# Kernel optimization log

Measured on AMD Instinct MI355X. Metric: run time of the kernel, lower is better.

Reference implementation:

```python
import jax, jax.numpy as jnp
import numpy as np

B, N, DIM = 4, 1024, 512
H, DH = 8, 64
INNER = H * DH
MLP = 2048
EPS = 1e-5


def layernorm(x, g, b):
    m = x.mean(-1, keepdims=True)
    v = ((x - m) ** 2).mean(-1, keepdims=True)
    return (x - m) / jnp.sqrt(v + EPS) * g + b


def setup_inputs() -> dict:
    key = jax.random.key(0)
    ks = jax.random.split(key, 12)
    s = 0.02
    return {
        "q": jax.random.normal(ks[0], (B, N, DIM), jnp.float32),
        "k": jax.random.normal(ks[1], (B, N, DIM), jnp.float32),
        "v": jax.random.normal(ks[2], (B, N, DIM), jnp.float32),
        "Win": jax.random.normal(ks[3], (INNER, DIM), jnp.float32) * s,
        "Wout": jax.random.normal(ks[4], (DIM, INNER), jnp.float32) * s,
        "bout": jnp.zeros((DIM,), jnp.float32),
        "g1": jnp.ones((DIM,), jnp.float32),
        "b1n": jnp.zeros((DIM,), jnp.float32),
        "g2": jnp.ones((DIM,), jnp.float32),
        "b2n": jnp.zeros((DIM,), jnp.float32),
        "Wup": jax.random.normal(ks[5], (MLP, DIM), jnp.float32) * s,
        "bup": jnp.zeros((MLP,), jnp.float32),
        "Wdn": jax.random.normal(ks[6], (DIM, MLP), jnp.float32) * s,
        "bdn": jnp.zeros((DIM,), jnp.float32),
        "wp_W1": jax.random.normal(ks[7], (DH, 2 * DH), jnp.float32) * s,
        "wp_b1": jnp.zeros((DH,), jnp.float32),
        "wp_g": jnp.ones((DH,), jnp.float32),
        "wp_b": jnp.zeros((DH,), jnp.float32),
        "wp_W2": jax.random.normal(ks[8], (3, DH), jnp.float32) * s,
        "wp_b2": jnp.zeros((3,), jnp.float32),
        "num_heads": H,
        "dim_head": DH,
        "mlp_dim": MLP,
    }


def reference(q, k, v, Win, Wout, bout, g1, b1n, g2, b2n, Wup, bup, Wdn, bdn,
              wp_W1, wp_b1, wp_g, wp_b, wp_W2, wp_b2, num_heads, dim_head, mlp_dim):
    b, n, _ = q.shape

    def split_heads(x):  # [b,n,dim] -> [h,b,n,d]
        f = x @ Win.T
        return f.reshape(b, n, num_heads, dim_head).transpose(2, 0, 1, 3)

    fq = split_heads(layernorm(q, g1, b1n))
    fk = split_heads(layernorm(k, g1, b1n))
    fv = split_heads(layernorm(v, g1, b1n))

    # cosine similarity component
    dots = jnp.einsum('hbnd,hbmd->hbnm', fq, fk)
    nq = jnp.linalg.norm(fq, axis=-1)  # [h,b,n]
    nk = jnp.linalg.norm(fk, axis=-1)  # [h,b,m]
    cosine_sim = dots / (nq[..., :, None] * nk[..., None, :])

    # mean-centered covariance component
    qc = fq - fq.mean(-1, keepdims=True)
    kc = fk - fk.mean(-1, keepdims=True)
    cov_component = jnp.einsum('hbnd,hbmd->hbnm', qc, kc) / dim_head

    # variance outer-product component (torch.var -> unbiased, ddof=1)
    qv = jnp.var(fq, axis=-1, ddof=1)  # [h,b,n]
    kv = jnp.var(fk, axis=-1, ddof=1)  # [h,b,m]
    var_component = qv[..., :, None] * kv[..., None, :] / dim_head

    # dynamic per-head mixing weights
    qg = fq.mean(axis=(1, 2))  # [h,d]
    kg = fk.mean(axis=(1, 2))
    feats = jnp.concatenate([qg, kg], axis=-1)  # [h,2d]
    h1 = jax.nn.relu(layernorm(feats @ wp_W1.T + wp_b1, wp_g, wp_b))
    w = jax.nn.softmax(h1 @ wp_W2.T + wp_b2, axis=-1)  # [h,3]
    cw = w[:, 0][:, None, None, None]
    covw = w[:, 1][:, None, None, None]
    vw = w[:, 2][:, None, None, None]

    scores = cw * cosine_sim + covw * cov_component + vw * var_component
    out = jnp.einsum('hbnm,hbmd->hbnd', scores, fv)
    out = out.transpose(1, 2, 0, 3).reshape(b, n, num_heads * dim_head)
    attn = out @ Wout.T + bout

    q2 = q + attn
    x = layernorm(q2, g2, b2n)
    y = jax.nn.gelu(x @ Wup.T + bup, approximate=False) @ Wdn.T + bdn
    return q2 + y
```

## Files before the change

kernel.cpp:

```cpp
#include <hip/hip_runtime.h>
#include <math.h>

#define EPS 1e-5f
#define ROWS 4096

typedef __attribute__((ext_vector_type(8))) short short8;
typedef __attribute__((ext_vector_type(4))) float floatx4;

__device__ inline short f2bf(float f) {
    unsigned u = __builtin_bit_cast(unsigned, f);
    unsigned r = (u + 0x7fffu + ((u >> 16) & 1u)) >> 16;
    return (short)r;
}

__global__ __launch_bounds__(256) void prep(
    const float* __restrict__ q, const float* __restrict__ k,
    const float* __restrict__ v, const float* __restrict__ g,
    const float* __restrict__ bb, short* __restrict__ qkvout,
    const float* __restrict__ w0, const float* __restrict__ w1,
    const float* __restrict__ w2, const float* __restrict__ w3,
    short* __restrict__ o0, short* __restrict__ o1,
    short* __restrict__ o2, short* __restrict__ o3,
    float* __restrict__ zero0) {
    int bx = blockIdx.x;
    int t = threadIdx.x;
    if (bx < 3072) {
        int tensor = bx >> 10;
        int xb = bx & 1023;
        const float* x = tensor == 0 ? q : (tensor == 1 ? k : v);
        int row = xb * 4 + (t >> 6);
        int col = (t & 63) * 8;
        const float* xr = x + (size_t)row * 512 + col;
        float4 v0 = *(const float4*)xr;
        float4 v1 = *(const float4*)(xr + 4);
        float s = v0.x + v0.y + v0.z + v0.w + v1.x + v1.y + v1.z + v1.w;
        float sq = v0.x * v0.x + v0.y * v0.y + v0.z * v0.z + v0.w * v0.w +
                   v1.x * v1.x + v1.y * v1.y + v1.z * v1.z + v1.w * v1.w;
#pragma unroll
        for (int off = 32; off; off >>= 1) {
            s += __shfl_xor(s, off);
            sq += __shfl_xor(sq, off);
        }
        float m = s * (1.f / 512.f);
        float rstd = rsqrtf(sq * (1.f / 512.f) - m * m + EPS);
        float4 g0 = *(const float4*)(g + col);
        float4 g1 = *(const float4*)(g + col + 4);
        float4 b0 = *(const float4*)(bb + col);
        float4 b1 = *(const float4*)(bb + col + 4);
        short8 o;
        o[0] = f2bf((v0.x - m) * rstd * g0.x + b0.x);
        o[1] = f2bf((v0.y - m) * rstd * g0.y + b0.y);
        o[2] = f2bf((v0.z - m) * rstd * g0.z + b0.z);
        o[3] = f2bf((v0.w - m) * rstd * g0.w + b0.w);
        o[4] = f2bf((v1.x - m) * rstd * g1.x + b1.x);
        o[5] = f2bf((v1.y - m) * rstd * g1.y + b1.y);
        o[6] = f2bf((v1.z - m) * rstd * g1.z + b1.z);
        o[7] = f2bf((v1.w - m) * rstd * g1.w + b1.w);
        *(short8*)(qkvout + (size_t)(tensor * 4096 + row) * 512 + col) = o;
        return;
    }
    if (bx < 4352) {
        int wb = bx - 3072;
        const float* src;
        short* dst;
        int base;
        if (wb < 128) { src = w0; dst = o0; base = wb; }
        else if (wb < 256) { src = w1; dst = o1; base = wb - 128; }
        else if (wb < 768) { src = w2; dst = o2; base = wb - 256; }
        else { src = w3; dst = o3; base = wb - 768; }
        int idx = base * 2048 + t * 8;
        float4 v0 = *(const float4*)(src + idx);
        float4 v1 = *(const float4*)(src + idx + 4);
        short8 o;
        o[0] = f2bf(v0.x); o[1] = f2bf(v0.y); o[2] = f2bf(v0.z); o[3] = f2bf(v0.w);
        o[4] = f2bf(v1.x); o[5] = f2bf(v1.y); o[6] = f2bf(v1.z); o[7] = f2bf(v1.w);
        *(short8*)(dst + idx) = o;
        return;
    }
    int zi = (bx - 4352) * 1024 + t * 4;
    if (zi < 267264) *(float4*)(zero0 + zi) = (float4){0.f, 0.f, 0.f, 0.f};
}

template <int TM, int TN, int EPI, bool OUT_BF16>
__global__ __launch_bounds__(256) void mfma_gemm_nt(
    const short* __restrict__ A, const short* __restrict__ B,
    void* __restrict__ C, int M, int N, int K,
    const float* __restrict__ bias, const float* __restrict__ resid,
    float* __restrict__ Sb, float* __restrict__ qgp, float* __restrict__ kgp) {
    constexpr int FI = TM / 32;
    constexpr int FJ = TN / 32;
    __shared__ short As[2][TM * 32];
    __shared__ short Bs[2][TN * 32];
    int t = threadIdx.x;
    int m0 = blockIdx.y * TM, n0 = blockIdx.x * TN;
    int w = t >> 6, lane = t & 63;
    int wm = (w & 1) * (TM / 2), wn = (w >> 1) * (TN / 2);
    floatx4 acc[FI][FJ];
#pragma unroll
    for (int i = 0; i < FI; ++i)
#pragma unroll
        for (int j = 0; j < FJ; ++j) acc[i][j] = (floatx4){0.f, 0.f, 0.f, 0.f};

    int arow = t >> 2, acol = (t & 3) * 8;
    const short* Ag = A + (size_t)(m0 + arow) * K + acol;
    const short* Bg = B + (size_t)(n0 + arow) * K + acol;
    int ldsbase = w * 1024;

    auto stage = [&](int k0, int buf) {
#pragma unroll
        for (int u = 0; u < TM / 64; ++u)
            __builtin_amdgcn_global_load_lds(
                (const __attribute__((address_space(1))) void*)(Ag + (size_t)u * 64 * K + k0),
                (__attribute__((address_space(3))) void*)((char*)As[buf] + u * 4096 + ldsbase),
                16, 0, 0);
#pragma unroll
        for (int u = 0; u < TN / 64; ++u)
            __builtin_amdgcn_global_load_lds(
                (const __attribute__((address_space(1))) void*)(Bg + (size_t)u * 64 * K + k0),
                (__attribute__((address_space(3))) void*)((char*)Bs[buf] + u * 4096 + ldsbase),
                16, 0, 0);
    };

    stage(0, 0);
    __syncthreads();
    int nsteps = K >> 5;
    for (int ks = 0; ks < nsteps; ++ks) {
        int buf = ks & 1;
        if (ks + 1 < nsteps) stage((ks + 1) << 5, buf ^ 1);
        int krow = (lane >> 4) * 8;
        short8 af[FI], bf[FJ];
#pragma unroll
        for (int i = 0; i < FI; ++i)
            af[i] = *(const short8*)&As[buf][(wm + i * 16 + (lane & 15)) * 32 + krow];
#pragma unroll
        for (int j = 0; j < FJ; ++j)
            bf[j] = *(const short8*)&Bs[buf][(wn + j * 16 + (lane & 15)) * 32 + krow];
#pragma unroll
        for (int i = 0; i < FI; ++i)
#pragma unroll
            for (int j = 0; j < FJ; ++j)
                acc[i][j] = __builtin_amdgcn_mfma_f32_16x16x32_bf16(
                    af[i], bf[j], acc[i][j], 0, 0, 0);
        __syncthreads();
    }

    int col = lane & 15, rbase = (lane >> 4) * 4;
#pragma unroll
    for (int i = 0; i < FI; ++i) {
#pragma unroll
        for (int j = 0; j < FJ; ++j) {
            int gcol = n0 + wn + j * 16 + col;
#pragma unroll
            for (int r = 0; r < 4; ++r) {
                int grow = m0 + wm + i * 16 + rbase + r;
                float v = acc[i][j][r];
                if (EPI == 2) v += bias[gcol] + resid[(size_t)grow * N + gcol];
                if (EPI == 3) {
                    v += bias[gcol];
                    v = 0.5f * v * (1.f + erff(v * 0.70710678118654752f));
                }
                if (OUT_BF16)
                    ((short*)C)[(size_t)grow * N + gcol] = f2bf(v);
                else
                    ((float*)C)[(size_t)grow * N + gcol] = v;
            }
        }
    }

    if (EPI == 1) {
        if (m0 < 8192) {
            int tensor = m0 >> 12;
            float* Sbase = Sb + (size_t)tensor * 98304;
            float* dst = tensor ? kgp : qgp;
            int head = (n0 + wn) >> 6;
            int rowbase = (m0 & 4095) + wm;
#pragma unroll
            for (int i = 0; i < FI; ++i) {
#pragma unroll
                for (int r = 0; r < 4; ++r) {
                    float s = 0.f, sq = 0.f;
#pragma unroll
                    for (int j = 0; j < FJ; ++j) {
                        float vv = acc[i][j][r];
                        s += vv;
                        sq += vv * vv;
                    }
#pragma unroll
                    for (int off = 1; off < 16; off <<= 1) {
                        s += __shfl_xor(s, off);
                        sq += __shfl_xor(sq, off);
                    }
                    if ((lane & 15) == 0) {
                        int row = rowbase + i * 16 + rbase + r;
                        int idx = head * ROWS + row;
                        float m = s * (1.f / 64.f);
                        Sbase[idx] = m;
                        Sbase[32768 + idx] = rsqrtf(sq);
                        Sbase[65536 + idx] = (sq - 64.f * m * m) * (1.f / 63.f);
                    }
                }
            }
            float cs[FJ];
#pragma unroll
            for (int j = 0; j < FJ; ++j) {
                float s = 0.f;
#pragma unroll
                for (int i = 0; i < FI; ++i)
#pragma unroll
                    for (int r = 0; r < 4; ++r) s += acc[i][j][r];
                s += __shfl_xor(s, 16);
                s += __shfl_xor(s, 32);
                cs[j] = s;
            }
            if (lane < 16) {
#pragma unroll
                for (int j = 0; j < FJ; ++j)
                    atomicAdd(&dst[head * 64 + j * 16 + lane], cs[j] * (1.f / 4096.f));
            }
        }
    }
}

__global__ __launch_bounds__(256) void lnconv(
    const float* __restrict__ x, const float* __restrict__ g,
    const float* __restrict__ bb, short* __restrict__ out) {
    int t = threadIdx.x;
    int row = blockIdx.x * 4 + (t >> 6);
    int col = (t & 63) * 8;
    const float* xr = x + (size_t)row * 512 + col;
    float4 v0 = *(const float4*)xr;
    float4 v1 = *(const float4*)(xr + 4);
    float s = v0.x + v0.y + v0.z + v0.w + v1.x + v1.y + v1.z + v1.w;
    float sq = v0.x * v0.x + v0.y * v0.y + v0.z * v0.z + v0.w * v0.w +
               v1.x * v1.x + v1.y * v1.y + v1.z * v1.z + v1.w * v1.w;
#pragma unroll
    for (int off = 32; off; off >>= 1) {
        s += __shfl_xor(s, off);
        sq += __shfl_xor(sq, off);
    }
    float m = s * (1.f / 512.f);
    float rstd = rsqrtf(sq * (1.f / 512.f) - m * m + EPS);
    float4 g0 = *(const float4*)(g + col);
    float4 g1 = *(const float4*)(g + col + 4);
    float4 b0 = *(const float4*)(bb + col);
    float4 b1 = *(const float4*)(bb + col + 4);
    short8 o;
    o[0] = f2bf((v0.x - m) * rstd * g0.x + b0.x);
    o[1] = f2bf((v0.y - m) * rstd * g0.y + b0.y);
    o[2] = f2bf((v0.z - m) * rstd * g0.z + b0.z);
    o[3] = f2bf((v0.w - m) * rstd * g0.w + b0.w);
    o[4] = f2bf((v1.x - m) * rstd * g1.x + b1.x);
    o[5] = f2bf((v1.y - m) * rstd * g1.y + b1.y);
    o[6] = f2bf((v1.z - m) * rstd * g1.z + b1.z);
    o[7] = f2bf((v1.w - m) * rstd * g1.w + b1.w);
    *(short8*)(out + (size_t)row * 512 + col) = o;
}

__global__ __launch_bounds__(256) void tr_kv(
    const float* __restrict__ fk, const float* __restrict__ fv,
    const float* __restrict__ rnk, const float* __restrict__ kvv,
    const float* __restrict__ mkm, short* __restrict__ fkTall,
    short* __restrict__ fvT, float* __restrict__ Sv,
    const float* __restrict__ qg, const float* __restrict__ kg,
    const float* __restrict__ W1, const float* __restrict__ b1,
    const float* __restrict__ g, const float* __restrict__ bb,
    const float* __restrict__ W2, const float* __restrict__ b2,
    float* __restrict__ wmix) {
    int hb = blockIdx.x;
    int t = threadIdx.x;
    if (blockIdx.y == 8) {
        if (blockIdx.z != 0 || hb >= 8 || t >= 64) return;
        int h = hb, j = t;
        float acc = 0.f;
        const float* w1r = W1 + j * 128;
        for (int i = 0; i < 64; ++i) acc += qg[h * 64 + i] * w1r[i];
        for (int i = 0; i < 64; ++i) acc += kg[h * 64 + i] * w1r[64 + i];
        acc += b1[j];
        float s = acc, sq = acc * acc;
#pragma unroll
        for (int off = 32; off; off >>= 1) {
            s += __shfl_xor(s, off);
            sq += __shfl_xor(sq, off);
        }
        float m = s * (1.f / 64.f);
        float var = sq * (1.f / 64.f) - m * m;
        float xh = (acc - m) * rsqrtf(var + EPS) * g[j] + bb[j];
        float r = fmaxf(xh, 0.f);
        float l[3];
#pragma unroll
        for (int c = 0; c < 3; ++c) {
            float p = r * W2[c * 64 + j];
#pragma unroll
            for (int off = 32; off; off >>= 1) p += __shfl_xor(p, off);
            l[c] = p + b2[c];
        }
        if (j == 0) {
            float mx = fmaxf(l[0], fmaxf(l[1], l[2]));
            float e0 = expf(l[0] - mx), e1 = expf(l[1] - mx), e2 = expf(l[2] - mx);
            float inv = 1.f / (e0 + e1 + e2);
            wmix[h * 3 + 0] = e0 * inv;
            wmix[h * 3 + 1] = e1 * inv;
            wmix[h * 3 + 2] = e2 * inv;
        }
        return;
    }
    int chunk = blockIdx.y;
    int tensor = blockIdx.z;
    int h = hb >> 2, b = hb & 3;
    __shared__ float tile[32][68];
    __shared__ float sc[32], sc2[32];
    const float* src = tensor ? fv : fk;
    float skv_acc = 0.f, smk_acc = 0.f;
    int e = t & 63, qd = t >> 6;
    int d = t >> 2, mg = (t & 3) * 8;
    for (int s4 = 0; s4 < 4; ++s4) {
        int m0 = chunk * 128 + s4 * 32;
        __syncthreads();
#pragma unroll
        for (int u = 0; u < 2; ++u) {
            int idx = u * 1024 + t * 4;
            int mm = idx >> 6, dd = idx & 63;
            *(float4*)&tile[mm][dd] =
                *(const float4*)&src[(size_t)(b * 1024 + m0 + mm) * 512 + h * 64 + dd];
        }
        if (t < 32) {
            int sidx = h * ROWS + b * 1024 + m0 + t;
            if (tensor == 0) {
                sc[t] = rnk[sidx];
            } else {
                sc[t] = kvv[sidx];
                sc2[t] = mkm[sidx];
            }
        }
        __syncthreads();
        if (tensor == 0) {
            short8 o1, o2;
#pragma unroll
            for (int i = 0; i < 8; ++i) {
                float vv = tile[mg + i][d];
                o1[i] = f2bf(vv);
                o2[i] = f2bf(vv * sc[mg + i]);
            }
            *(short8*)&fkTall[((size_t)hb * 128 + d) * 1024 + m0 + mg] = o1;
            *(short8*)&fkTall[((size_t)hb * 128 + 64 + d) * 1024 + m0 + mg] = o2;
        } else {
            short8 o1;
#pragma unroll
            for (int i = 0; i < 8; ++i) o1[i] = f2bf(tile[mg + i][d]);
            *(short8*)&fvT[((size_t)hb * 64 + d) * 1024 + m0 + mg] = o1;
#pragma unroll
            for (int i = 0; i < 8; ++i) {
                float vv = tile[qd * 8 + i][e];
                skv_acc += sc[qd * 8 + i] * vv;
                smk_acc += sc2[qd * 8 + i] * vv;
            }
        }
    }
    if (tensor == 1) {
        atomicAdd(&Sv[hb * 128 + e], skv_acc);
        atomicAdd(&Sv[hb * 128 + 64 + e], smk_acc);
    }
}

__global__ __launch_bounds__(256) void kside_gemm(
    const short* __restrict__ fkTall, const short* __restrict__ fvT,
    float* __restrict__ Mnew) {
    int hb = blockIdx.x, half = blockIdx.y, kz = blockIdx.z;
    const short* A = fkTall + ((size_t)hb * 128 + half * 64) * 1024 + kz * 256;
    const short* B = fvT + (size_t)hb * 64 * 1024 + kz * 256;
    __shared__ short As[2][64 * 32];
    __shared__ short Bs[2][64 * 32];
    int t = threadIdx.x;
    int w = t >> 6, lane = t & 63;
    int wm = (w & 1) * 32, wn = (w >> 1) * 32;
    floatx4 acc[2][2];
#pragma unroll
    for (int i = 0; i < 2; ++i)
#pragma unroll
        for (int j = 0; j < 2; ++j) acc[i][j] = (floatx4){0.f, 0.f, 0.f, 0.f};
    int arow = t >> 2, acol = (t & 3) * 8;
    const short* Ag = A + (size_t)arow * 1024 + acol;
    const short* Bg = B + (size_t)arow * 1024 + acol;
    int ldsbase = w * 1024;

    auto stage = [&](int k0, int buf) {
        __builtin_amdgcn_global_load_lds(
            (const __attribute__((address_space(1))) void*)(Ag + k0),
            (__attribute__((address_space(3))) void*)((char*)As[buf] + ldsbase), 16, 0, 0);
        __builtin_amdgcn_global_load_lds(
            (const __attribute__((address_space(1))) void*)(Bg + k0),
            (__attribute__((address_space(3))) void*)((char*)Bs[buf] + ldsbase), 16, 0, 0);
    };

    stage(0, 0);
    __syncthreads();
    for (int ks = 0; ks < 8; ++ks) {
        int buf = ks & 1;
        if (ks + 1 < 8) stage((ks + 1) << 5, buf ^ 1);
        int krow = (lane >> 4) * 8;
        short8 af[2], bf[2];
#pragma unroll
        for (int i = 0; i < 2; ++i)
            af[i] = *(const short8*)&As[buf][(wm + i * 16 + (lane & 15)) * 32 + krow];
#pragma unroll
        for (int j = 0; j < 2; ++j)
            bf[j] = *(const short8*)&Bs[buf][(wn + j * 16 + (lane & 15)) * 32 + krow];
#pragma unroll
        for (int i = 0; i < 2; ++i)
#pragma unroll
            for (int j = 0; j < 2; ++j)
                acc[i][j] = __builtin_amdgcn_mfma_f32_16x16x32_bf16(
                    af[i], bf[j], acc[i][j], 0, 0, 0);
        __syncthreads();
    }
    int col = lane & 15, rbase = (lane >> 4) * 4;
    float* Cb = Mnew + (size_t)hb * 8192 + half * 4096;
#pragma unroll
    for (int i = 0; i < 2; ++i)
#pragma unroll
        for (int j = 0; j < 2; ++j)
#pragma unroll
            for (int r = 0; r < 4; ++r)
                atomicAdd(&Cb[(wm + i * 16 + rbase + r) * 64 + wn + j * 16 + col],
                          acc[i][j][r]);
}

__global__ __launch_bounds__(256) void qside(
    const float* __restrict__ fq, const float* __restrict__ Mnew,
    const float* __restrict__ Sv, const float* __restrict__ rnq,
    const float* __restrict__ mq, const float* __restrict__ qv,
    const float* __restrict__ wmix, short* __restrict__ attn_out) {
    int ntile = blockIdx.x, hb = blockIdx.y;
    int h = hb >> 2, b = hb & 3;
    __shared__ float M1s[4096], M2s[4096], fqt[4096];
    __shared__ float Skvs[64], Smks[64], rnqs[64], mqs[64], qvs[64];
    int t = threadIdx.x;
    const float* base = Mnew + (size_t)hb * 8192;
#pragma unroll
    for (int u = 0; u < 4; ++u) {
        int idx = t * 4 + u * 1024;
        *(float4*)&M2s[idx] = *(const float4*)&base[idx];
        *(float4*)&M1s[idx] = *(const float4*)&base[4096 + idx];
    }
    int n0 = ntile * 64;
#pragma unroll
    for (int u = 0; u < 4; ++u) {
        int idx = t * 4 + u * 1024;
        int r = idx >> 6, d = idx & 63;
        *(float4*)&fqt[idx] = *(const float4*)&fq[(size_t)(b * 1024 + n0 + r) * 512 + h * 64 + d];
    }
    if (t < 64) {
        Skvs[t] = Sv[hb * 128 + t];
        Smks[t] = Sv[hb * 128 + 64 + t];
        int sidx = h * ROWS + b * 1024 + n0 + t;
        rnqs[t] = rnq[sidx];
        mqs[t] = mq[sidx];
        qvs[t] = qv[sidx];
    }
    __syncthreads();
    float cw = wmix[h * 3 + 0], covw = wmix[h * 3 + 1], vw = wmix[h * 3 + 2];
    int e = t & 63, rq = t >> 6;
    float a1[16] = {}, a2[16] = {};
    for (int d4 = 0; d4 < 64; d4 += 4) {
        float md1[4], md2[4];
#pragma unroll
        for (int dd = 0; dd < 4; ++dd) {
            md1[dd] = M1s[(d4 + dd) * 64 + e];
            md2[dd] = M2s[(d4 + dd) * 64 + e];
        }
#pragma unroll
        for (int i = 0; i < 16; ++i) {
            float4 f = *(const float4*)&fqt[(rq * 16 + i) * 64 + d4];
            a1[i] += f.x * md1[0] + f.y * md1[1] + f.z * md1[2] + f.w * md1[3];
            a2[i] += f.x * md2[0] + f.y * md2[1] + f.z * md2[2] + f.w * md2[3];
        }
    }
    float c2 = covw * (1.f / 64.f), c3 = vw * (1.f / 64.f);
#pragma unroll
    for (int i = 0; i < 16; ++i) {
        int rr = rq * 16 + i;
        float v = cw * rnqs[rr] * a1[i] + c2 * a2[i] + c3 * qvs[rr] * Skvs[e] -
                  covw * mqs[rr] * Smks[e];
        attn_out[(size_t)(b * 1024 + n0 + rr) * 512 + h * 64 + e] = f2bf(v);
    }
}

extern "C" void kernel_launch(void* const* d_in, const int* in_sizes, int n_in,
                              void* d_out, int out_size, void* d_ws, size_t ws_size,
                              hipStream_t stream) {
    const float* q = (const float*)d_in[0];
    const float* k = (const float*)d_in[1];
    const float* v = (const float*)d_in[2];
    const float* Win = (const float*)d_in[3];
    const float* Wout = (const float*)d_in[4];
    const float* bout = (const float*)d_in[5];
    const float* g1 = (const float*)d_in[6];
    const float* b1n = (const float*)d_in[7];
    const float* g2 = (const float*)d_in[8];
    const float* b2n = (const float*)d_in[9];
    const float* Wup = (const float*)d_in[10];
    const float* bup = (const float*)d_in[11];
    const float* Wdn = (const float*)d_in[12];
    const float* bdn = (const float*)d_in[13];
    const float* wpW1 = (const float*)d_in[14];
    const float* wpb1 = (const float*)d_in[15];
    const float* wpg = (const float*)d_in[16];
    const float* wpb = (const float*)d_in[17];
    const float* wpW2 = (const float*)d_in[18];
    const float* wpb2 = (const float*)d_in[19];
    float* out = (float*)d_out;

    float* wsf = (float*)d_ws;
    float* fq = wsf;
    float* fk = wsf + 2097152;
    float* fv = wsf + 2 * 2097152;
    short* hmid = (short*)wsf;
    short* qkvln = (short*)(wsf + 6291456);
    short* fkTall = (short*)(wsf + 6291456);
    short* fvT = (short*)(wsf + 8388608);
    short* attnbf = (short*)(wsf + 6291456);
    short* x2bf = (short*)(wsf + 6291456 + 1048576);
    short* Winbf = (short*)(wsf + 9437184);
    short* Woutbf = (short*)(wsf + 9437184 + 131072);
    short* Wupbf = (short*)(wsf + 9437184 + 262144);
    short* Wdnbf = (short*)(wsf + 9437184 + 262144 + 524288);
    float* S = wsf + 10747904;
    float* qg = S + 196608;
    float* kg = qg + 512;
    float* Mnew = kg + 512;
    float* Sv = Mnew + 262144;
    float* wmix = Sv + 4096;
    float* mqS = S, *rnqS = S + 32768, *qvS = S + 65536;
    float* mkS = S + 98304, *rnkS = S + 131072, *kvS = S + 163840;

    prep<<<4613, 256, 0, stream>>>(q, k, v, g1, b1n, qkvln,
                                   Win, Wout, Wup, Wdn,
                                   Winbf, Woutbf, Wupbf, Wdnbf, qg);

    mfma_gemm_nt<64, 128, 1, false><<<dim3(4, 192), 256, 0, stream>>>(
        qkvln, Winbf, fq, 12288, 512, 512, nullptr, nullptr, S, qg, kg);

    tr_kv<<<dim3(32, 9, 2), 256, 0, stream>>>(fk, fv, rnkS, kvS, mkS,
                                              fkTall, fvT, Sv,
                                              qg, kg, wpW1, wpb1, wpg, wpb,
                                              wpW2, wpb2, wmix);

    kside_gemm<<<dim3(32, 2, 4), 256, 0, stream>>>(fkTall, fvT, Mnew);

    qside<<<dim3(16, 32), 256, 0, stream>>>(fq, Mnew, Sv, rnqS, mqS, qvS,
                                            wmix, attnbf);

    mfma_gemm_nt<64, 64, 2, false><<<dim3(8, 64), 256, 0, stream>>>(
        attnbf, Woutbf, out, 4096, 512, 512, bout, q, nullptr, nullptr, nullptr);

    lnconv<<<1024, 256, 0, stream>>>(out, g2, b2n, x2bf);
    mfma_gemm_nt<64, 128, 3, true><<<dim3(16, 64), 256, 0, stream>>>(
        x2bf, Wupbf, hmid, 4096, 2048, 512, bup, nullptr, nullptr, nullptr, nullptr);
    mfma_gemm_nt<64, 128, 2, false><<<dim3(4, 64), 256, 0, stream>>>(
        hmid, Wdnbf, out, 4096, 512, 2048, bdn, out, nullptr, nullptr, nullptr);
}
```

Measured before the change: 233.0 us.

## Fold second layernorm into Wup GEMM and store QKV projections as bf16

Removes the separate lnconv kernel. The Wout GEMM epilogue now writes a bf16 copy of q2 and atomically accumulates per-row sum and sum-of-squares. The Wup GEMM applies the layernorm algebraically: it uses g2-scaled Wup weights and precomputed Wg/Bn vectors, and corrects with rstd and mean in the epilogue. The QKV projection output is also stored as bf16 instead of fp32, halving traffic for tr_kv and qside. The risks are extra precision loss, since the statistics come from fp32 values while the GEMM input is a bf16 un-normalized q2, and atomic contention on the row statistics.

```diff
diff --git a/kernel.cpp b/kernel.cpp
--- a/kernel.cpp
+++ b/kernel.cpp
@@ -11,6 +11,9 @@
     unsigned u = __builtin_bit_cast(unsigned, f);
     unsigned r = (u + 0x7fffu + ((u >> 16) & 1u)) >> 16;
     return (short)r;
+}
+__device__ inline float bf2f(short s) {
+    return __builtin_bit_cast(float, (unsigned)(unsigned short)s << 16);
 }
 
 __global__ __launch_bounds__(256) void prep(
@@ -21,6 +24,8 @@
     const float* __restrict__ w2, const float* __restrict__ w3,
     short* __restrict__ o0, short* __restrict__ o1,
     short* __restrict__ o2, short* __restrict__ o3,
+    const float* __restrict__ g2, const float* __restrict__ b2n,
+    float* __restrict__ Bn, float* __restrict__ Wg,
     float* __restrict__ zero0) {
     int bx = blockIdx.x;
     int t = threadIdx.x;
@@ -61,12 +66,42 @@
     }
     if (bx < 4352) {
         int wb = bx - 3072;
+        if (wb >= 256 && wb < 768) {
+            int base = wb - 256;
+            int idx = base * 2048 + t * 8;
+            int n = idx >> 9, c = idx & 511;
+            float4 v0 = *(const float4*)(w2 + idx);
+            float4 v1 = *(const float4*)(w2 + idx + 4);
+            float4 ga = *(const float4*)(g2 + c);
+            float4 gb = *(const float4*)(g2 + c + 4);
+            float4 ba = *(const float4*)(b2n + c);
+            float4 bbv = *(const float4*)(b2n + c + 4);
+            short8 o;
+            o[0] = f2bf(ga.x * v0.x); o[1] = f2bf(ga.y * v0.y);
+            o[2] = f2bf(ga.z * v0.z); o[3] = f2bf(ga.w * v0.w);
+            o[4] = f2bf(gb.x * v1.x); o[5] = f2bf(gb.y * v1.y);
+            o[6] = f2bf(gb.z * v1.z); o[7] = f2bf(gb.w * v1.w);
+            *(short8*)(o2 + idx) = o;
+            float bn = ba.x * v0.x + ba.y * v0.y + ba.z * v0.z + ba.w * v0.w +
+                       bbv.x * v1.x + bbv.y * v1.y + bbv.z * v1.z + bbv.w * v1.w;
+            float wg = ga.x * v0.x + ga.y * v0.y + ga.z * v0.z + ga.w * v0.w +
+                       gb.x * v1.x + gb.y * v1.y + gb.z * v1.z + gb.w * v1.w;
+#pragma unroll
+            for (int off = 32; off; off >>= 1) {
+                bn += __shfl_xor(bn, off);
+                wg += __shfl_xor(wg, off);
+            }
+            if ((t & 63) == 0) {
+                Bn[n] = bn;
+                Wg[n] = wg;
+            }
+            return;
+        }
         const float* src;
         short* dst;
         int base;
         if (wb < 128) { src = w0; dst = o0; base = wb; }
         else if (wb < 256) { src = w1; dst = o1; base = wb - 128; }
-        else if (wb < 768) { src = w2; dst = o2; base = wb - 256; }
         else { src = w3; dst = o3; base = wb - 768; }
         int idx = base * 2048 + t * 8;
         float4 v0 = *(const float4*)(src + idx);
@@ -78,7 +113,7 @@
         return;
     }
     int zi = (bx - 4352) * 1024 + t * 4;
-    if (zi < 267264) *(float4*)(zero0 + zi) = (float4){0.f, 0.f, 0.f, 0.f};
+    if (zi < 275456) *(float4*)(zero0 + zi) = (float4){0.f, 0.f, 0.f, 0.f};
 }
 
 template <int TM, int TN, int EPI, bool OUT_BF16>
@@ -86,7 +121,8 @@
     const short* __restrict__ A, const short* __restrict__ B,
     void* __restrict__ C, int M, int N, int K,
     const float* __restrict__ bias, const float* __restrict__ resid,
-    float* __restrict__ Sb, float* __restrict__ qgp, float* __restrict__ kgp) {
+    short* __restrict__ C2, float* __restrict__ Sb,
+    float* __restrict__ qgp, float* __restrict__ kgp) {
     constexpr int FI = TM / 32;
     constexpr int FJ = TN / 32;
     __shared__ short As[2][TM * 32];
@@ -145,29 +181,74 @@
     }
 
     int col = lane & 15, rbase = (lane >> 4) * 4;
-#pragma unroll
-    for (int i = 0; i < FI; ++i) {
-#pragma unroll
-        for (int j = 0; j < FJ; ++j) {
-            int gcol = n0 + wn + j * 16 + col;
+    if constexpr (EPI == 5) {
+#pragma unroll
+        for (int i = 0; i < FI; ++i) {
 #pragma unroll
             for (int r = 0; r < 4; ++r) {
                 int grow = m0 + wm + i * 16 + rbase + r;
-                float v = acc[i][j][r];
-                if (EPI == 2) v += bias[gcol] + resid[(size_t)grow * N + gcol];
-                if (EPI == 3) {
-                    v += bias[gcol];
-                    v = 0.5f * v * (1.f + erff(v * 0.70710678118654752f));
+                float s = 0.f, sq = 0.f;
+#pragma unroll
+                for (int j = 0; j < FJ; ++j) {
+                    int gcol = n0 + wn + j * 16 + col;
+                    float vv = acc[i][j][r] + bias[gcol] +
+                               resid[(size_t)grow * N + gcol];
+                    ((float*)C)[(size_t)grow * N + gcol] = vv;
+                    C2[(size_t)grow * N + gcol] = f2bf(vv);
+                    s += vv;
+                    sq += vv * vv;
                 }
-                if (OUT_BF16)
-                    ((short*)C)[(size_t)grow * N + gcol] = f2bf(v);
-                else
-                    ((float*)C)[(size_t)grow * N + gcol] = v;
-            }
-        }
-    }
-
-    if (EPI == 1) {
+#pragma unroll
+                for (int off = 1; off < 16; off <<= 1) {
+                    s += __shfl_xor(s, off);
+                    sq += __shfl_xor(sq, off);
+                }
+                if ((lane & 15) == 0) {
+                    atomicAdd(&Sb[grow], s);
+                    atomicAdd(&Sb[4096 + grow], sq);
+                }
+            }
+        }
+    } else if constexpr (EPI == 4) {
+#pragma unroll
+        for (int i = 0; i < FI; ++i) {
+#pragma unroll
+            for (int r = 0; r < 4; ++r) {
+                int grow = m0 + wm + i * 16 + rbase + r;
+                float m = Sb[grow] * (1.f / 512.f);
+                float rstd = rsqrtf(Sb[4096 + grow] * (1.f / 512.f) - m * m + EPS);
+                float mrstd = m * rstd;
+#pragma unroll
+                for (int j = 0; j < FJ; ++j) {
+                    int gcol = n0 + wn + j * 16 + col;
+                    float vv = rstd * acc[i][j][r] + qgp[gcol] + bias[gcol] -
+                               mrstd * kgp[gcol];
+                    vv = 0.5f * vv * (1.f + erff(vv * 0.70710678118654752f));
+                    ((short*)C)[(size_t)grow * N + gcol] = f2bf(vv);
+                }
+            }
+        }
+    } else {
+#pragma unroll
+        for (int i = 0; i < FI; ++i) {
+#pragma unroll
+            for (int j = 0; j < FJ; ++j) {
+                int gcol = n0 + wn + j * 16 + col;
+#pragma unroll
+                for (int r = 0; r < 4; ++r) {
+                    int grow = m0 + wm + i * 16 + rbase + r;
+                    float v = acc[i][j][r];
+                    if (EPI == 2) v += bias[gcol] + resid[(size_t)grow * N + gcol];
+                    if (OUT_BF16)
+                        ((short*)C)[(size_t)grow * N + gcol] = f2bf(v);
+                    else
+                        ((float*)C)[(size_t)grow * N + gcol] = v;
+                }
+            }
+        }
+    }
+
+    if constexpr (EPI == 1) {
         if (m0 < 8192) {
             int tensor = m0 >> 12;
             float* Sbase = Sb + (size_t)tensor * 98304;
@@ -221,43 +302,8 @@
     }
 }
 
-__global__ __launch_bounds__(256) void lnconv(
-    const float* __restrict__ x, const float* __restrict__ g,
-    const float* __restrict__ bb, short* __restrict__ out) {
-    int t = threadIdx.x;
-    int row = blockIdx.x * 4 + (t >> 6);
-    int col = (t & 63) * 8;
-    const float* xr = x + (size_t)row * 512 + col;
-    float4 v0 = *(const float4*)xr;
-    float4 v1 = *(const float4*)(xr + 4);
-    float s = v0.x + v0.y + v0.z + v0.w + v1.x + v1.y + v1.z + v1.w;
-    float sq = v0.x * v0.x + v0.y * v0.y + v0.z * v0.z + v0.w * v0.w +
-               v1.x * v1.x + v1.y * v1.y + v1.z * v1.z + v1.w * v1.w;
-#pragma unroll
-    for (int off = 32; off; off >>= 1) {
-        s += __shfl_xor(s, off);
-        sq += __shfl_xor(sq, off);
-    }
-    float m = s * (1.f / 512.f);
-    float rstd = rsqrtf(sq * (1.f / 512.f) - m * m + EPS);
-    float4 g0 = *(const float4*)(g + col);
-    float4 g1 = *(const float4*)(g + col + 4);
-    float4 b0 = *(const float4*)(bb + col);
-    float4 b1 = *(const float4*)(bb + col + 4);
-    short8 o;
-    o[0] = f2bf((v0.x - m) * rstd * g0.x + b0.x);
-    o[1] = f2bf((v0.y - m) * rstd * g0.y + b0.y);
-    o[2] = f2bf((v0.z - m) * rstd * g0.z + b0.z);
-    o[3] = f2bf((v0.w - m) * rstd * g0.w + b0.w);
-    o[4] = f2bf((v1.x - m) * rstd * g1.x + b1.x);
-    o[5] = f2bf((v1.y - m) * rstd * g1.y + b1.y);
-    o[6] = f2bf((v1.z - m) * rstd * g1.z + b1.z);
-    o[7] = f2bf((v1.w - m) * rstd * g1.w + b1.w);
-    *(short8*)(out + (size_t)row * 512 + col) = o;
-}
-
 __global__ __launch_bounds__(256) void tr_kv(
-    const float* __restrict__ fk, const float* __restrict__ fv,
+    const short* __restrict__ fkb, const short* __restrict__ fvb,
     const float* __restrict__ rnk, const float* __restrict__ kvv,
     const float* __restrict__ mkm, short* __restrict__ fkTall,
     short* __restrict__ fvT, float* __restrict__ Sv,
@@ -309,19 +355,19 @@
     int h = hb >> 2, b = hb & 3;
     __shared__ float tile[32][68];
     __shared__ float sc[32], sc2[32];
-    const float* src = tensor ? fv : fk;
+    const short* src = tensor ? fvb : fkb;
     float skv_acc = 0.f, smk_acc = 0.f;
     int e = t & 63, qd = t >> 6;
     int d = t >> 2, mg = (t & 3) * 8;
     for (int s4 = 0; s4 < 4; ++s4) {
         int m0 = chunk * 128 + s4 * 32;
         __syncthreads();
-#pragma unroll
-        for (int u = 0; u < 2; ++u) {
-            int idx = u * 1024 + t * 4;
+        {
+            int idx = t * 8;
             int mm = idx >> 6, dd = idx & 63;
-            *(float4*)&tile[mm][dd] =
-                *(const float4*)&src[(size_t)(b * 1024 + m0 + mm) * 512 + h * 64 + dd];
+            short8 sv = *(const short8*)&src[(size_t)(b * 1024 + m0 + mm) * 512 + h * 64 + dd];
+#pragma unroll
+            for (int i = 0; i < 8; ++i) tile[mm][dd + i] = bf2f(sv[i]);
         }
         if (t < 32) {
             int sidx = h * ROWS + b * 1024 + m0 + t;
@@ -426,7 +472,7 @@
 }
 
 __global__ __launch_bounds__(256) void qside(
-    const float* __restrict__ fq, const float* __restrict__ Mnew,
+    const short* __restrict__ fqb, const float* __restrict__ Mnew,
     const float* __restrict__ Sv, const float* __restrict__ rnq,
     const float* __restrict__ mq, const float* __restrict__ qv,
     const float* __restrict__ wmix, short* __restrict__ attn_out) {
@@ -444,10 +490,12 @@
     }
     int n0 = ntile * 64;
 #pragma unroll
-    for (int u = 0; u < 4; ++u) {
-        int idx = t * 4 + u * 1024;
+    for (int u = 0; u < 2; ++u) {
+        int idx = t * 8 + u * 2048;
         int r = idx >> 6, d = idx & 63;
-        *(float4*)&fqt[idx] = *(const float4*)&fq[(size_t)(b * 1024 + n0 + r) * 512 + h * 64 + d];
+        short8 sv = *(const short8*)&fqb[(size_t)(b * 1024 + n0 + r) * 512 + h * 64 + d];
+#pragma unroll
+        for (int i = 0; i < 8; ++i) fqt[idx + i] = bf2f(sv[i]);
     }
     if (t < 64) {
         Skvs[t] = Sv[hb * 128 + t];
@@ -511,51 +559,59 @@
     float* out = (float*)d_out;
 
     float* wsf = (float*)d_ws;
-    float* fq = wsf;
-    float* fk = wsf + 2097152;
-    float* fv = wsf + 2 * 2097152;
+    short* fqkv = (short*)wsf;
+    short* fkb = fqkv + (size_t)4096 * 512;
+    short* fvb = fqkv + (size_t)8192 * 512;
+    short* qkvln = (short*)(wsf + 3145728);
     short* hmid = (short*)wsf;
-    short* qkvln = (short*)(wsf + 6291456);
-    short* fkTall = (short*)(wsf + 6291456);
-    short* fvT = (short*)(wsf + 8388608);
-    short* attnbf = (short*)(wsf + 6291456);
-    short* x2bf = (short*)(wsf + 6291456 + 1048576);
-    short* Winbf = (short*)(wsf + 9437184);
-    short* Woutbf = (short*)(wsf + 9437184 + 131072);
-    short* Wupbf = (short*)(wsf + 9437184 + 262144);
-    short* Wdnbf = (short*)(wsf + 9437184 + 262144 + 524288);
-    float* S = wsf + 10747904;
+    short* fkTall = (short*)(wsf + 4194304);
+    short* attnbf = (short*)(wsf + 4194304);
+    short* fvT = (short*)(wsf + 6291456);
+    short* q2bf = (short*)(wsf + 7340032);
+    short* Winbf = (short*)(wsf + 8388608);
+    short* Woutbf = (short*)(wsf + 8388608 + 131072);
+    short* Wupbf = (short*)(wsf + 8388608 + 262144);
+    short* Wdnbf = (short*)(wsf + 8388608 + 262144 + 524288);
+    float* S = wsf + 9699328;
     float* qg = S + 196608;
     float* kg = qg + 512;
     float* Mnew = kg + 512;
     float* Sv = Mnew + 262144;
-    float* wmix = Sv + 4096;
+    float* rowstats = Sv + 4096;
+    float* wmix = rowstats + 8192;
+    float* Bn = wmix + 32;
+    float* Wg = Bn + 2048;
     float* mqS = S, *rnqS = S + 32768, *qvS = S + 65536;
     float* mkS = S + 98304, *rnkS = S + 131072, *kvS = S + 163840;
 
-    prep<<<4613, 256, 0, stream>>>(q, k, v, g1, b1n, qkvln,
+    prep<<<4621, 256, 0, stream>>>(q, k, v, g1, b1n, qkvln,
                                    Win, Wout, Wup, Wdn,
-                                   Winbf, Woutbf, Wupbf, Wdnbf, qg);
-
-    mfma_gemm_nt<64, 128, 1, false><<<dim3(4, 192), 256, 0, stream>>>(
-        qkvln, Winbf, fq, 12288, 512, 512, nullptr, nullptr, S, qg, kg);
-
-    tr_kv<<<dim3(32, 9, 2), 256, 0, stream>>>(fk, fv, rnkS, kvS, mkS,
+                                   Winbf, Woutbf, Wupbf, Wdnbf,
+                                   g2, b2n, Bn, Wg, qg);
+
+    mfma_gemm_nt<64, 128, 1, true><<<dim3(4, 192), 256, 0, stream>>>(
+        qkvln, Winbf, fqkv, 12288, 512, 512, nullptr, nullptr, nullptr,
+        S, qg, kg);
+
+    tr_kv<<<dim3(32, 9, 2), 256, 0, stream>>>(fkb, fvb, rnkS, kvS, mkS,
                                               fkTall, fvT, Sv,
                                               qg, kg, wpW1, wpb1, wpg, wpb,
                                               wpW2, wpb2, wmix);
 
     kside_gemm<<<dim3(32, 2, 4), 256, 0, stream>>>(fkTall, fvT, Mnew);
 
-    qside<<<dim3(16, 32), 256, 0, stream>>>(fq, Mnew, Sv, rnqS, mqS, qvS,
+    qside<<<dim3(16, 32), 256, 0, stream>>>(fqkv, Mnew, Sv, rnqS, mqS, qvS,
                                             wmix, attnbf);
 
-    mfma_gemm_nt<64, 64, 2, false><<<dim3(8, 64), 256, 0, stream>>>(
-        attnbf, Woutbf, out, 4096, 512, 512, bout, q, nullptr, nullptr, nullptr);
-
-    lnconv<<<1024, 256, 0, stream>>>(out, g2, b2n, x2bf);
-    mfma_gemm_nt<64, 128, 3, true><<<dim3(16, 64), 256, 0, stream>>>(
-        x2bf, Wupbf, hmid, 4096, 2048, 512, bup, nullptr, nullptr, nullptr, nullptr);
+    mfma_gemm_nt<64, 64, 5, false><<<dim3(8, 64), 256, 0, stream>>>(
+        attnbf, Woutbf, out, 4096, 512, 512, bout, q, q2bf,
+        rowstats, nullptr, nullptr);
+
+    mfma_gemm_nt<64, 128, 4, true><<<dim3(16, 64), 256, 0, stream>>>(
+        q2bf, Wupbf, hmid, 4096, 2048, 512, bup, nullptr, nullptr,
+        rowstats, Bn, Wg);
+
     mfma_gemm_nt<64, 128, 2, false><<<dim3(4, 64), 256, 0, stream>>>(
-        hmid, Wdnbf, out, 4096, 512, 2048, bdn, out, nullptr, nullptr, nullptr);
-}
+        hmid, Wdnbf, out, 4096, 512, 2048, bdn, out, nullptr,
+        nullptr, nullptr, nullptr);
+}
```

New measurement: 233.7 us. No clear change (+0.3%).
